# Performance work log

Measured on AMD Instinct MI355X. Metric: run time of the kernel, lower is better.

Reference implementation:

```python
import jax, jax.numpy as jnp
import numpy as np

N_NODES = 100000
N_EDGES = 3200000
IN_FEATS = 512
HIDDEN = 64
N_CLASSES = 32


def setup_inputs() -> dict:
    key = jax.random.key(0)
    k1, k2, k3, k4 = jax.random.split(key, 4)
    x = jax.random.normal(k1, (N_NODES, IN_FEATS), dtype=jnp.float32)
    edge_index = jax.random.randint(k2, (2, N_EDGES), 0, N_NODES, dtype=jnp.int64)
    # Glorot-ish init for weights
    W1 = jax.random.normal(k3, (IN_FEATS, HIDDEN), dtype=jnp.float32) / np.sqrt(IN_FEATS)
    b1 = jnp.zeros((HIDDEN,), dtype=jnp.float32)
    W2 = jax.random.normal(k4, (HIDDEN, N_CLASSES), dtype=jnp.float32) / np.sqrt(HIDDEN)
    b2 = jnp.zeros((N_CLASSES,), dtype=jnp.float32)
    return {"x": x, "edge_index": edge_index, "W1": W1, "b1": b1, "W2": W2, "b2": b2}


def reference(x, edge_index, W1, b1, W2, b2):
    N = x.shape[0]
    # GCNConv default: add self-loops, unit edge weights (edge_attr is None for Cora)
    loop = jnp.arange(N, dtype=edge_index.dtype)
    src = jnp.concatenate([edge_index[0], loop])  # [E+N]
    dst = jnp.concatenate([edge_index[1], loop])  # [E+N]
    w = jnp.ones(src.shape[0], dtype=x.dtype)
    # symmetric normalization: deg^-1/2[src] * w * deg^-1/2[dst]
    deg = jax.ops.segment_sum(w, dst, num_segments=N)
    dinv = jnp.where(deg > 0, jax.lax.rsqrt(deg), 0.0)
    norm = dinv[src] * w * dinv[dst]  # [E+N]

    def gcn_layer(h, W, b):
        h = h @ W                              # transform first (out dim small)
        msg = h[src] * norm[:, None]           # gather + scale  [E+N, d_out]
        agg = jax.ops.segment_sum(msg, dst, num_segments=N)  # scatter-add
        return agg + b

    h = jax.nn.relu(gcn_layer(x, W1, b1))
    # F.dropout(training=self.training) -> identity in eval mode
    out = gcn_layer(h, W2, b2)
    return jax.nn.log_softmax(out, axis=1)
```

## Files before the change

### kernel.cpp

```cpp
#include <hip/hip_runtime.h>
#include <hip/hip_fp16.h>
#include <math.h>

constexpr int N_NODES = 100000;
constexpr int N_EDGES = 3200000;
constexpr int IN_F = 512;
constexpr int HID = 64;
constexpr int NCLS = 32;
constexpr int CAP = 80;
constexpr int SHIFT = 9;
constexpr int NB = 196;
constexpr int BCAPC = 16976;
constexpr int CHUNK = 8192;
constexpr int SENT = N_NODES;

constexpr int GEMM1_BLOCKS = (N_NODES + 63) / 64;
constexpr int PART_BLOCKS  = (N_EDGES + CHUNK - 1) / CHUNK;

typedef short short8 __attribute__((ext_vector_type(8)));
typedef float f32x4 __attribute__((ext_vector_type(4)));
typedef int intx4 __attribute__((ext_vector_type(4)));

__device__ __forceinline__ unsigned short f2bf(float f) {
    union { float f; unsigned int u; } v; v.f = f;
    unsigned int r = (v.u + 0x7fffu + ((v.u >> 16) & 1u)) >> 16;
    return (unsigned short)r;
}
__device__ __forceinline__ float bf2f(unsigned short h) {
    union { unsigned int u; float f; } v; v.u = ((unsigned int)h) << 16;
    return v.f;
}
__device__ __forceinline__ unsigned char f2e5(float f) {
    unsigned short u = __half_as_ushort(__float2half(f));
    return (unsigned char)((u + 0x7Fu + ((u >> 8) & 1u)) >> 8);
}
__device__ __forceinline__ float e52f(unsigned char b) {
    return __half2float(__ushort_as_half((unsigned short)((unsigned short)b << 8)));
}

__global__ __launch_bounds__(256) void k_prep(const float* __restrict__ W1,
                                              unsigned short* __restrict__ W1T,
                                              unsigned char* __restrict__ h1s,
                                              unsigned char* __restrict__ h2s,
                                              int* __restrict__ gtail) {
    if (blockIdx.x == 128) {
        int t = threadIdx.x;
        if (t < HID)  h1s[(size_t)SENT * HID + t] = 0;
        if (t < NCLS) h2s[(size_t)SENT * NCLS + t] = 0;
        for (int i = t; i < NB * 16; i += 256) gtail[i] = 0;
        return;
    }
    int t = blockIdx.x * 256 + threadIdx.x;
    int k = t >> 6, c = t & 63;
    W1T[(size_t)c * IN_F + k] = f2bf(W1[(size_t)k * HID + c]);
}


__global__ __launch_bounds__(512) void k_part(const int* __restrict__ src,
                                              const int* __restrict__ dst,
                                              int* __restrict__ gtail,
                                              int* __restrict__ recs) {
    __shared__ alignas(16) char smem[47168];
    int* buf            = (int*)smem;
    unsigned char* bbuf = (unsigned char*)(smem + 32768);
    int* loc   = (int*)(smem + 40960);
    int* lh    = (int*)(smem + 43012);
    int* lbase = (int*)(smem + 45060);
    int* wsum  = (int*)(smem + 47108);
    const int tid = threadIdx.x;
    const int lane = tid & 63;
    const int wv = tid >> 6;
    const int c0 = blockIdx.x * CHUNK;
    const int cnum = min(CHUNK, N_EDGES - c0);
    lh[tid] = 0;
    __syncthreads();
    int dd[16], ss[16], rk[16];
    #pragma unroll
    for (int k = 0; k < 16; ++k) {
        int i = k * 512 + tid;
        if (i < cnum) {
            dd[k] = dst[c0 + i];
            ss[k] = src[c0 + i];
            rk[k] = atomicAdd(&lh[dd[k] >> SHIFT], 1);
        }
    }
    __syncthreads();
    int orig = lh[tid];
    int v = orig;
    #pragma unroll
    for (int off = 1; off < 64; off <<= 1) {
        int t = __shfl_up(v, off, 64);
        if (lane >= off) v += t;
    }
    if (lane == 63) wsum[wv] = v;
    __syncthreads();
    int pre = 0;
    #pragma unroll
    for (int k = 0; k < 8; ++k) if (k < wv) pre += wsum[k];
    int incl = v + pre;
    loc[tid] = incl - orig;
    if (tid < NB && orig > 0) lbase[tid] = atomicAdd(&gtail[tid * 16], orig);
    __syncthreads();
    #pragma unroll
    for (int k = 0; k < 16; ++k) {
        int i = k * 512 + tid;
        if (i < cnum) {
            int b = dd[k] >> SHIFT;
            int pos = loc[b] + rk[k];
            buf[pos] = ((dd[k] & 511) << 17) | ss[k];
            bbuf[pos] = (unsigned char)b;
        }
    }
    __syncthreads();
    for (int i = tid; i < cnum; i += 512) {
        int b = bbuf[i];
        int idx = lbase[b] + (i - loc[b]);
        if (idx < BCAPC) recs[(size_t)b * BCAPC + idx] = buf[i];
    }
}


__global__ __launch_bounds__(256) void k_gemm1(const float* __restrict__ x,
                                               const unsigned short* __restrict__ W1T,
                                               unsigned short* __restrict__ h1) {
    __shared__ alignas(16) char smem[20608];
    const int tid = threadIdx.x;
    const int lane = tid & 63;
    short* Xb = (short*)smem;
    short* Wb = (short*)(smem + 10240);
    const int row0 = blockIdx.x * 64;
    const int w = tid >> 6;
    const int r0l = (w >> 1) * 32;
    const int c0l = (w & 1) * 32;
    const int lrow = lane & 15;
    const int lkb = (lane >> 4) << 3;
    const int sr = tid >> 2;
    const int skq = (tid & 3) << 3;
    f32x4 acc00 = {0.f, 0.f, 0.f, 0.f}, acc01 = acc00, acc10 = acc00, acc11 = acc00;

    const int grow = row0 + sr;
    const bool valid = grow < N_NODES;
    const float* xp0 = &x[(size_t)grow * IN_F + skq];
    const unsigned short* wp0 = &W1T[(size_t)sr * IN_F + skq];

    float4 v0 = make_float4(0.f, 0.f, 0.f, 0.f), v1 = v0;
    if (valid) { v0 = *reinterpret_cast<const float4*>(xp0);
                 v1 = *reinterpret_cast<const float4*>(xp0 + 4); }
    short8 wa = *reinterpret_cast<const short8*>(wp0);

    #pragma unroll 4
    for (int s = 0; s < 16; ++s) {
        const int p = (s & 1) * 2560;
        short8 px;
        px[0] = (short)f2bf(v0.x); px[1] = (short)f2bf(v0.y);
        px[2] = (short)f2bf(v0.z); px[3] = (short)f2bf(v0.w);
        px[4] = (short)f2bf(v1.x); px[5] = (short)f2bf(v1.y);
        px[6] = (short)f2bf(v1.z); px[7] = (short)f2bf(v1.w);
        *reinterpret_cast<short8*>(&Xb[p + sr * 40 + skq]) = px;
        *reinterpret_cast<short8*>(&Wb[p + sr * 40 + skq]) = wa;
        __syncthreads();
        if (s < 15) {
            const float* xp = xp0 + (s + 1) * 32;
            if (valid) { v0 = *reinterpret_cast<const float4*>(xp);
                         v1 = *reinterpret_cast<const float4*>(xp + 4); }
            wa = *reinterpret_cast<const short8*>(wp0 + (s + 1) * 32);
        }
        short8 a0 = *reinterpret_cast<const short8*>(&Xb[p + (r0l + lrow) * 40 + lkb]);
        short8 a1 = *reinterpret_cast<const short8*>(&Xb[p + (r0l + 16 + lrow) * 40 + lkb]);
        short8 b0 = *reinterpret_cast<const short8*>(&Wb[p + (c0l + lrow) * 40 + lkb]);
        short8 b1 = *reinterpret_cast<const short8*>(&Wb[p + (c0l + 16 + lrow) * 40 + lkb]);
        acc00 = __builtin_amdgcn_mfma_f32_16x16x32_bf16(a0, b0, acc00, 0, 0, 0);
        acc01 = __builtin_amdgcn_mfma_f32_16x16x32_bf16(a0, b1, acc01, 0, 0, 0);
        acc10 = __builtin_amdgcn_mfma_f32_16x16x32_bf16(a1, b0, acc10, 0, 0, 0);
        acc11 = __builtin_amdgcn_mfma_f32_16x16x32_bf16(a1, b1, acc11, 0, 0, 0);
    }
    const int vr0 = row0 + r0l + ((lane >> 4) << 2);
    const int gc0 = c0l + (lane & 15);
    #pragma unroll
    for (int v = 0; v < 4; ++v) {
        int gr = vr0 + v;
        if (gr < N_NODES) {
            h1[(size_t)gr * HID + gc0]      = f2bf(acc00[v]);
            h1[(size_t)gr * HID + gc0 + 16] = f2bf(acc01[v]);
        }
        int gr2 = gr + 16;
        if (gr2 < N_NODES) {
            h1[(size_t)gr2 * HID + gc0]      = f2bf(acc10[v]);
            h1[(size_t)gr2 * HID + gc0 + 16] = f2bf(acc11[v]);
        }
    }
}


__global__ __launch_bounds__(1024) void k_phase2(const int* __restrict__ gtail,
                                                 const int* __restrict__ recs,
                                                 int* __restrict__ slots,
                                                 int* __restrict__ cnt,
                                                 float* __restrict__ dinv,
                                                 const unsigned short* __restrict__ h1,
                                                 unsigned char* __restrict__ h1s) {
    __shared__ int scnt[512];
    const int b = blockIdx.x;
    const int tid = threadIdx.x;
    if (tid < 512) scnt[tid] = 0;
    __syncthreads();
    int nrec = min(gtail[b * 16], BCAPC);
    const int* rb = recs + (size_t)b * BCAPC;
    for (int i = tid; i < nrec; i += 1024) {
        int r = rb[i];
        int ln = r >> 17;
        int s  = r & 0x1FFFF;
        int p = atomicAdd(&scnt[ln], 1);
        int node = (b << SHIFT) + ln;
        if (p < CAP) slots[(size_t)node * CAP + p] = s;
    }
    __syncthreads();
    if (tid < 512) {
        int node = (b << SHIFT) + tid;
        if (node < N_NODES) {
            int c = scnt[tid];
            cnt[node] = c;
            dinv[node] = rsqrtf(1.0f + (float)c);
            int c2 = min(c, CAP);
            int degp = (c2 + 15) & ~15;
            for (int p = c2; p < degp; ++p) slots[(size_t)node * CAP + p] = SENT;
        }
    }
    for (int idx = tid; idx < 512 * 8; idx += 1024) {
        int ln = idx >> 3, g = idx & 7;
        int node = (b << SHIFT) + ln;
        if (node >= N_NODES) continue;
        float dv = rsqrtf(1.0f + (float)scnt[ln]);
        const unsigned short* hr = h1 + (size_t)node * HID;
        unsigned char* hs = h1s + (size_t)node * HID;
        short8 hv = *reinterpret_cast<const short8*>(hr + g * 8);
        unsigned int lo = 0, hi = 0;
        #pragma unroll
        for (int e = 0; e < 4; ++e)
            lo |= (unsigned int)f2e5(bf2f((unsigned short)hv[e]) * dv) << (e * 8);
        #pragma unroll
        for (int e = 0; e < 4; ++e)
            hi |= (unsigned int)f2e5(bf2f((unsigned short)hv[4 + e]) * dv) << (e * 8);
        *reinterpret_cast<uint2*>(hs + g * 8) = make_uint2(lo, hi);
    }
}


__global__ __launch_bounds__(256) void k_gather1(const int* __restrict__ cnt,
                                                 const int* __restrict__ slots,
                                                 const float* __restrict__ dinv,
                                                 const unsigned char* __restrict__ h1s,
                                                 const float* __restrict__ b1,
                                                 const float* __restrict__ W2,
                                                 unsigned char* __restrict__ h2s) {
    __shared__ alignas(16) float hsh[4][64];
    const int lane = threadIdx.x & 63;
    const int wv = threadIdx.x >> 6;
    const int cls = lane & 31;
    const int half = lane >> 5;
    float w[32];
    #pragma unroll
    for (int j = 0; j < 32; ++j)
        w[j] = W2[(size_t)(half * 32 + j) * NCLS + cls];
    const float bb = b1[lane];
    const int nw = gridDim.x * 4;
    for (int n0 = blockIdx.x * 4 + wv; n0 < N_NODES; n0 += nw) {
        const int n = __builtin_amdgcn_readfirstlane(n0);
        float dn = dinv[n];
        int deg = min(cnt[n], CAP);
        int degp = (deg + 15) & ~15;
        size_t base = (size_t)n * CAP;
        float a0 = e52f(h1s[(((unsigned)n) << 6) + lane]);
        float a1 = 0.f, a2 = 0.f, a3 = 0.f, a4 = 0.f, a5 = 0.f, a6 = 0.f, a7 = 0.f;
        for (int j = 0; j < degp; j += 16) {
            intx4 sa = __builtin_nontemporal_load(reinterpret_cast<const intx4*>(&slots[base + j]));
            intx4 sb = __builtin_nontemporal_load(reinterpret_cast<const intx4*>(&slots[base + j + 4]));
            intx4 sc = __builtin_nontemporal_load(reinterpret_cast<const intx4*>(&slots[base + j + 8]));
            intx4 sd = __builtin_nontemporal_load(reinterpret_cast<const intx4*>(&slots[base + j + 12]));
            a0 += e52f(h1s[(((unsigned)sa.x) << 6) + lane]);
            a1 += e52f(h1s[(((unsigned)sa.y) << 6) + lane]);
            a2 += e52f(h1s[(((unsigned)sa.z) << 6) + lane]);
            a3 += e52f(h1s[(((unsigned)sa.w) << 6) + lane]);
            a4 += e52f(h1s[(((unsigned)sb.x) << 6) + lane]);
            a5 += e52f(h1s[(((unsigned)sb.y) << 6) + lane]);
            a6 += e52f(h1s[(((unsigned)sb.z) << 6) + lane]);
            a7 += e52f(h1s[(((unsigned)sb.w) << 6) + lane]);
            a0 += e52f(h1s[(((unsigned)sc.x) << 6) + lane]);
            a1 += e52f(h1s[(((unsigned)sc.y) << 6) + lane]);
            a2 += e52f(h1s[(((unsigned)sc.z) << 6) + lane]);
            a3 += e52f(h1s[(((unsigned)sc.w) << 6) + lane]);
            a4 += e52f(h1s[(((unsigned)sd.x) << 6) + lane]);
            a5 += e52f(h1s[(((unsigned)sd.y) << 6) + lane]);
            a6 += e52f(h1s[(((unsigned)sd.z) << 6) + lane]);
            a7 += e52f(h1s[(((unsigned)sd.w) << 6) + lane]);
        }
        float v = fmaf(((a0 + a1) + (a2 + a3)) + ((a4 + a5) + (a6 + a7)), dn, bb);
        v = fmaxf(v, 0.f);
        hsh[wv][lane] = v;
        float acc = 0.f;
        #pragma unroll
        for (int q = 0; q < 8; ++q) {
            f32x4 hv = *reinterpret_cast<const f32x4*>(&hsh[wv][half * 32 + q * 4]);
            acc = fmaf(hv.x, w[q * 4 + 0], acc);
            acc = fmaf(hv.y, w[q * 4 + 1], acc);
            acc = fmaf(hv.z, w[q * 4 + 2], acc);
            acc = fmaf(hv.w, w[q * 4 + 3], acc);
        }
        acc += __shfl_xor(acc, 32, 64);
        if (half == 0)
            h2s[(((unsigned)n) << 5) + cls] = f2e5(acc * dn);
    }
}


__global__ __launch_bounds__(256) void k_out(const int* __restrict__ cnt,
                                             const int* __restrict__ slots,
                                             const float* __restrict__ dinv,
                                             const unsigned char* __restrict__ h2s,
                                             const float* __restrict__ b2,
                                             float* __restrict__ out) {
    int wid = blockIdx.x * 4 + (threadIdx.x >> 6);
    int n = __builtin_amdgcn_readfirstlane(wid);
    if (n >= N_NODES) return;
    int lane = threadIdx.x & 63;
    int cls = lane & 31;
    int half = lane >> 5;
    float dn = dinv[n];
    int deg = min(cnt[n], CAP);
    int degp = (deg + 15) & ~15;
    size_t base = (size_t)n * CAP;
    float a0 = half ? 0.f : e52f(h2s[(((unsigned)n) << 5) + cls]);
    float a1 = 0.f, a2 = 0.f, a3 = 0.f;
    for (int j = 0; j < degp; j += 16) {
        intx4 s0 = __builtin_nontemporal_load(
            reinterpret_cast<const intx4*>(&slots[base + j + half * 8]));
        intx4 s1 = __builtin_nontemporal_load(
            reinterpret_cast<const intx4*>(&slots[base + j + half * 8 + 4]));
        a0 += e52f(h2s[(((unsigned)s0.x) << 5) + cls]);
        a1 += e52f(h2s[(((unsigned)s0.y) << 5) + cls]);
        a2 += e52f(h2s[(((unsigned)s0.z) << 5) + cls]);
        a3 += e52f(h2s[(((unsigned)s0.w) << 5) + cls]);
        a0 += e52f(h2s[(((unsigned)s1.x) << 5) + cls]);
        a1 += e52f(h2s[(((unsigned)s1.y) << 5) + cls]);
        a2 += e52f(h2s[(((unsigned)s1.z) << 5) + cls]);
        a3 += e52f(h2s[(((unsigned)s1.w) << 5) + cls]);
    }
    float acc = (a0 + a1) + (a2 + a3);
    acc += __shfl_xor(acc, 32, 64);
    float z = fmaf(acc, dn, b2[cls]);
    float mx = z;
    #pragma unroll
    for (int d = 16; d > 0; d >>= 1) mx = fmaxf(mx, __shfl_xor(mx, d, 32));
    float ex = expf(z - mx);
    float sm = ex;
    #pragma unroll
    for (int d = 16; d > 0; d >>= 1) sm += __shfl_xor(sm, d, 32);
    if (half == 0)
        out[(size_t)n * NCLS + cls] = z - mx - logf(sm);
}


extern "C" void kernel_launch(void* const* d_in, const int* in_sizes, int n_in,
                              void* d_out, int out_size, void* d_ws, size_t ws_size,
                              hipStream_t stream) {
    const float* x  = (const float*)d_in[0];
    const int*   ei = (const int*)d_in[1];
    const float* W1 = (const float*)d_in[2];
    const float* b1 = (const float*)d_in[3];
    const float* W2 = (const float*)d_in[4];
    const float* b2 = (const float*)d_in[5];
    float* out = (float*)d_out;
    char* ws = (char*)d_ws;

    const int* src = ei;
    const int* dst = ei + N_EDGES;

    int*   gtail = (int*)ws;
    int*   cnt   = (int*)(ws + 16384);
    float* dinv  = (float*)(ws + 416384);
    unsigned short* W1T = (unsigned short*)(ws + 816384);
    int*   slots = (int*)(ws + 881920);
    unsigned short* h1 = (unsigned short*)(ws + 32882048ull);
    unsigned char* h1s = (unsigned char*)(ws + 45682048ull);
    char*  recs_base   = ws + 52082176ull;
    int*   recs  = (int*)recs_base;
    unsigned char* h2s  = (unsigned char*)(ws + 65391360ull);

    k_prep<<<129, 256, 0, stream>>>(W1, W1T, h1s, h2s, gtail);
    k_part<<<PART_BLOCKS, 512, 0, stream>>>(src, dst, gtail, recs);
    k_gemm1<<<GEMM1_BLOCKS, 256, 0, stream>>>(x, W1T, h1);
    k_phase2<<<NB, 1024, 0, stream>>>(gtail, recs, slots, cnt, dinv, h1, h1s);
    k_gather1<<<1536, 256, 0, stream>>>(cnt, slots, dinv, h1s, b1, W2, h2s);
    k_out<<<(N_NODES + 3) / 4, 256, 0, stream>>>(cnt, slots, dinv, h2s, b2, out);
}
```

Before: 199.0 us.

## Stage GEMM1 tiles via direct global-to-LDS loads with XOR swizzle

The first-layer GEMM now copies fp32 x tiles and bf16 W1T tiles straight from global memory into shared memory with global_load_lds, double-buffered across K steps, instead of loading into registers, converting, and storing. Conversion to bf16 moves to after the shared-memory read, and an XOR swizzle replaces row padding to avoid bank conflicts. This aims to cut register staging and VGPR pressure and to overlap the next tile's load with MFMA work. In exchange the fp32 tile doubles LDS traffic for x, and conversion is repeated per wave, since each wave converts its own A fragment.

```diff
diff --git a/kernel.cpp b/kernel.cpp
--- a/kernel.cpp
+++ b/kernel.cpp
@@ -36,6 +36,11 @@
 }
 __device__ __forceinline__ float e52f(unsigned char b) {
     return __half2float(__ushort_as_half((unsigned short)((unsigned short)b << 8)));
+}
+__device__ __forceinline__ void gload16(const void* g, void* l) {
+    __builtin_amdgcn_global_load_lds((const __attribute__((address_space(1))) unsigned int*)g,
+                                     (__attribute__((address_space(3))) unsigned int*)l,
+                                     16, 0, 0);
 }
 
 __global__ __launch_bounds__(256) void k_prep(const float* __restrict__ W1,
@@ -123,56 +128,76 @@
 __global__ __launch_bounds__(256) void k_gemm1(const float* __restrict__ x,
                                                const unsigned short* __restrict__ W1T,
                                                unsigned short* __restrict__ h1) {
-    __shared__ alignas(16) char smem[20608];
+    __shared__ alignas(16) char smem[24576];
+    float* Xf = (float*)smem;
+    unsigned short* Wf = (unsigned short*)(smem + 16384);
     const int tid = threadIdx.x;
     const int lane = tid & 63;
-    short* Xb = (short*)smem;
-    short* Wb = (short*)(smem + 10240);
     const int row0 = blockIdx.x * 64;
     const int w = tid >> 6;
     const int r0l = (w >> 1) * 32;
     const int c0l = (w & 1) * 32;
     const int lrow = lane & 15;
     const int lkb = (lane >> 4) << 3;
-    const int sr = tid >> 2;
-    const int skq = (tid & 3) << 3;
     f32x4 acc00 = {0.f, 0.f, 0.f, 0.f}, acc01 = acc00, acc10 = acc00, acc11 = acc00;
 
-    const int grow = row0 + sr;
-    const bool valid = grow < N_NODES;
-    const float* xp0 = &x[(size_t)grow * IN_F + skq];
-    const unsigned short* wp0 = &W1T[(size_t)sr * IN_F + skq];
-
-    float4 v0 = make_float4(0.f, 0.f, 0.f, 0.f), v1 = v0;
-    if (valid) { v0 = *reinterpret_cast<const float4*>(xp0);
-                 v1 = *reinterpret_cast<const float4*>(xp0 + 4); }
-    short8 wa = *reinterpret_cast<const short8*>(wp0);
-
-    #pragma unroll 4
+    const int rowA0 = tid >> 3;
+    const int rowA1 = 32 + (tid >> 3);
+    const int gA = tid & 7;
+    const float* srcX0 = x + (size_t)min(row0 + rowA0, N_NODES - 1) * IN_F + ((gA ^ (rowA0 & 7)) << 2);
+    const float* srcX1 = x + (size_t)min(row0 + rowA1, N_NODES - 1) * IN_F + ((gA ^ (rowA1 & 7)) << 2);
+    const int rowW = tid >> 2;
+    const int gW = tid & 3;
+    const unsigned short* srcW = W1T + (size_t)rowW * IN_F + ((gW ^ (rowW & 3)) << 3);
+    char* ldsX0 = smem + (w << 10);
+    char* ldsX1 = smem + 4096 + (w << 10);
+    char* ldsW  = smem + 16384 + (w << 10);
+
+    gload16(srcX0, ldsX0);
+    gload16(srcX1, ldsX1);
+    gload16(srcW,  ldsW);
+    __syncthreads();
+
+    const int RA = r0l + lrow, RA2 = RA + 16;
+    const int RB = c0l + lrow, RB2 = RB + 16;
+    const int qx = lkb >> 2;
+    const int qw = lkb >> 3;
+    const int sxA  = ((qx ^ (RA & 7)) << 2),  sxA_ = (((qx + 1) ^ (RA & 7)) << 2);
+    const int sxB  = ((qx ^ (RA2 & 7)) << 2), sxB_ = (((qx + 1) ^ (RA2 & 7)) << 2);
+    const int swB  = ((qw ^ (RB & 3)) << 3);
+    const int swB2 = ((qw ^ (RB2 & 3)) << 3);
+
+    #pragma unroll 2
     for (int s = 0; s < 16; ++s) {
-        const int p = (s & 1) * 2560;
-        short8 px;
-        px[0] = (short)f2bf(v0.x); px[1] = (short)f2bf(v0.y);
-        px[2] = (short)f2bf(v0.z); px[3] = (short)f2bf(v0.w);
-        px[4] = (short)f2bf(v1.x); px[5] = (short)f2bf(v1.y);
-        px[6] = (short)f2bf(v1.z); px[7] = (short)f2bf(v1.w);
-        *reinterpret_cast<short8*>(&Xb[p + sr * 40 + skq]) = px;
-        *reinterpret_cast<short8*>(&Wb[p + sr * 40 + skq]) = wa;
-        __syncthreads();
+        const int p = s & 1;
         if (s < 15) {
-            const float* xp = xp0 + (s + 1) * 32;
-            if (valid) { v0 = *reinterpret_cast<const float4*>(xp);
-                         v1 = *reinterpret_cast<const float4*>(xp + 4); }
-            wa = *reinterpret_cast<const short8*>(wp0 + (s + 1) * 32);
-        }
-        short8 a0 = *reinterpret_cast<const short8*>(&Xb[p + (r0l + lrow) * 40 + lkb]);
-        short8 a1 = *reinterpret_cast<const short8*>(&Xb[p + (r0l + 16 + lrow) * 40 + lkb]);
-        short8 b0 = *reinterpret_cast<const short8*>(&Wb[p + (c0l + lrow) * 40 + lkb]);
-        short8 b1 = *reinterpret_cast<const short8*>(&Wb[p + (c0l + 16 + lrow) * 40 + lkb]);
+            gload16(srcX0 + (s + 1) * 32, ldsX0 + (p ^ 1) * 8192);
+            gload16(srcX1 + (s + 1) * 32, ldsX1 + (p ^ 1) * 8192);
+            gload16(srcW  + (s + 1) * 32, ldsW  + (p ^ 1) * 4096);
+        }
+        const float* xrA = Xf + p * 2048 + RA * 32;
+        const float* xrB = Xf + p * 2048 + RA2 * 32;
+        f32x4 va0 = *(const f32x4*)(xrA + sxA);
+        f32x4 va1 = *(const f32x4*)(xrA + sxA_);
+        f32x4 vb0 = *(const f32x4*)(xrB + sxB);
+        f32x4 vb1 = *(const f32x4*)(xrB + sxB_);
+        const unsigned short* wr = Wf + p * 2048;
+        short8 b0 = *(const short8*)(wr + RB * 32 + swB);
+        short8 b1 = *(const short8*)(wr + RB2 * 32 + swB2);
+        short8 a0, a1;
+        a0[0] = (short)f2bf(va0[0]); a0[1] = (short)f2bf(va0[1]);
+        a0[2] = (short)f2bf(va0[2]); a0[3] = (short)f2bf(va0[3]);
+        a0[4] = (short)f2bf(va1[0]); a0[5] = (short)f2bf(va1[1]);
+        a0[6] = (short)f2bf(va1[2]); a0[7] = (short)f2bf(va1[3]);
+        a1[0] = (short)f2bf(vb0[0]); a1[1] = (short)f2bf(vb0[1]);
+        a1[2] = (short)f2bf(vb0[2]); a1[3] = (short)f2bf(vb0[3]);
+        a1[4] = (short)f2bf(vb1[0]); a1[5] = (short)f2bf(vb1[1]);
+        a1[6] = (short)f2bf(vb1[2]); a1[7] = (short)f2bf(vb1[3]);
         acc00 = __builtin_amdgcn_mfma_f32_16x16x32_bf16(a0, b0, acc00, 0, 0, 0);
         acc01 = __builtin_amdgcn_mfma_f32_16x16x32_bf16(a0, b1, acc01, 0, 0, 0);
         acc10 = __builtin_amdgcn_mfma_f32_16x16x32_bf16(a1, b0, acc10, 0, 0, 0);
         acc11 = __builtin_amdgcn_mfma_f32_16x16x32_bf16(a1, b1, acc11, 0, 0, 0);
+        __syncthreads();
     }
     const int vr0 = row0 + r0l + ((lane >> 4) << 2);
     const int gc0 = c0l + (lane & 15);
```

Result: no change. 200.0 us (+0.5%).
